# Kernel tuning notes

Hardware: AMD Instinct MI355X
Metric: run time of the kernel (lower is better)

The kernel has to match this reference:

```python
import jax, jax.numpy as jnp
import numpy as np

B, L = 4096, 200
N_USERS, N_ITEMS, N_CATS, N_DUR = 200000, 500000, 1000, 20
D = 64  # item_embed_dim == seq_embed_dim


def _lin(k, din, dout):
    kw, kb = jax.random.split(k)
    s = 1.0 / np.sqrt(din)
    return (jax.random.uniform(kw, (din, dout), minval=-s, maxval=s),
            jax.random.uniform(kb, (dout,), minval=-s, maxval=s))


def setup_inputs() -> dict:
    key = jax.random.key(0)
    ks = jax.random.split(key, 20)
    inp = {
        'user_id': jax.random.randint(ks[0], (B,), 0, N_USERS),
        'item_id': jax.random.randint(ks[1], (B,), 0, N_ITEMS),
        'item_category': jax.random.randint(ks[2], (B,), 0, N_CATS),
        'item_dur_bkt': jax.random.randint(ks[3], (B,), 0, N_DUR),
        'user_dense': jax.random.normal(ks[4], (B, 25), dtype=jnp.float32),
        'item_dense': jax.random.normal(ks[5], (B, 3), dtype=jnp.float32),
        'history_seq': jax.random.randint(ks[6], (B, L), 0, N_ITEMS + 1),
        # embedding tables (init std=0.01 as in _init_weights)
        'user_W': 0.01 * jax.random.normal(ks[7], (N_USERS, 64), dtype=jnp.float32),
        'item_W': 0.01 * jax.random.normal(ks[8], (N_ITEMS, D), dtype=jnp.float32),
        'cat_W': 0.01 * jax.random.normal(ks[9], (N_CATS, 16), dtype=jnp.float32),
        'dur_W': 0.01 * jax.random.normal(ks[10], (N_DUR, 8), dtype=jnp.float32),
        'hist_W': 0.01 * jax.random.normal(ks[11], (N_ITEMS + 1, D), dtype=jnp.float32),
    }
    # attention MLP: 4*D=256 -> 64 -> 32 -> 1
    inp['aW0'], inp['ab0'] = _lin(ks[12], 4 * D, 64)
    inp['aW1'], inp['ab1'] = _lin(ks[13], 64, 32)
    inp['aW2'], inp['ab2'] = _lin(ks[14], 32, 1)
    # final MLP: concat_dim 64+64+16+8+25+3+64 = 244 -> 256 -> 128 -> 1
    inp['mW0'], inp['mb0'] = _lin(ks[15], 244, 256)
    inp['mW1'], inp['mb1'] = _lin(ks[16], 256, 128)
    inp['mW2'], inp['mb2'] = _lin(ks[17], 128, 1)
    return inp


def reference(user_id, item_id, item_category, item_dur_bkt, user_dense, item_dense,
              history_seq, user_W, item_W, cat_W, dur_W, hist_W,
              aW0, ab0, aW1, ab1, aW2, ab2, mW0, mb0, mW1, mb1, mW2, mb2):
    u_emb = user_W[user_id]            # (B, 64)
    i_emb = item_W[item_id]            # (B, D)
    c_emb = cat_W[item_category]       # (B, 16)
    d_emb = dur_W[item_dur_bkt]        # (B, 8)
    hist = hist_W[history_seq]         # (B, L, D)

    t = i_emb[:, None, :]              # (B, 1, D); item_dim == seq_dim so no slice
    tb = jnp.broadcast_to(t, hist.shape)
    feat = jnp.concatenate([hist, tb, hist * t, hist - t], axis=-1)  # (B, L, 4D)

    h = jax.nn.relu(feat @ aW0 + ab0)
    h = jax.nn.relu(h @ aW1 + ab1)
    scores = (h @ aW2 + ab2)[..., 0]   # (B, L)

    pad_mask = history_seq == 0
    scores = jnp.where(pad_mask, jnp.float32(-1e9), scores)
    w = jax.nn.softmax(scores, axis=-1)                # (B, L)
    pooled = jnp.einsum('bl,bld->bd', w, hist)         # (B, D)

    x = jnp.concatenate([u_emb, i_emb, c_emb, d_emb, user_dense, item_dense, pooled], axis=-1)
    h = jax.nn.relu(x @ mW0 + mb0)     # dropout is identity in eval mode
    h = jax.nn.relu(h @ mW1 + mb1)
    logit = (h @ mW2 + mb2)[..., 0]
    return jax.nn.sigmoid(logit)       # (B,)
```

## Files before the change

### kernel.cpp

```cpp
#include <hip/hip_runtime.h>
#include <hip/hip_bf16.h>

#define L_SZ 200
#define RB 8
#define HS_STRIDE 72

typedef __attribute__((ext_vector_type(8))) short short8;
typedef __attribute__((ext_vector_type(4))) float floatx4;

__device__ __forceinline__ unsigned short f2bf(float f) {
    unsigned int u = __float_as_uint(f);
    unsigned int r = (u + 0x7fffu + ((u >> 16) & 1u)) >> 16;
    return (unsigned short)r;
}
__device__ __forceinline__ float bf2f(unsigned short h) {
    return __uint_as_float(((unsigned int)h) << 16);
}
__device__ __forceinline__ float wave_sum64(float v) {
    #pragma unroll
    for (int m = 1; m <= 32; m <<= 1) v += __shfl_xor(v, m, 64);
    return v;
}
__device__ __forceinline__ float wave_max64(float v) {
    #pragma unroll
    for (int m = 1; m <= 32; m <<= 1) v = fmaxf(v, __shfl_xor(v, m, 64));
    return v;
}
__device__ __forceinline__ unsigned int pk2(float a, float b) {
    return ((unsigned int)f2bf(b) << 16) | (unsigned int)f2bf(a);
}

__global__ __launch_bounds__(256, 4) void attn_kernel(
    const int* __restrict__ item_id, const int* __restrict__ hist_seq,
    const float* __restrict__ item_W, const float* __restrict__ hist_W,
    const float* __restrict__ aW0, const float* __restrict__ ab0,
    const float* __restrict__ aW1, const float* __restrict__ ab1,
    const float* __restrict__ aW2, const float* __restrict__ ab2,
    float* __restrict__ pooled_ws)
{
    __shared__ __align__(16) unsigned char smem[39136];
    unsigned short* Hs  = (unsigned short*)(smem);
    unsigned short* BB  = (unsigned short*)(smem + 28800);
    int*   seq_sh = (int*)(smem + 36992);
    float* scores = (float*)(smem + 37792);
    float* iemb   = (float*)(smem + 38592);
    float* cb     = (float*)(smem + 38848);
    float* red    = (float*)(smem + 39104);

    const int tid  = threadIdx.x;
    const int w    = tid >> 6;
    const int lane = tid & 63;
    const int b    = blockIdx.x;
    const int* hseq = hist_seq + b * L_SZ;

    if (tid < 64)   iemb[tid]   = item_W[(size_t)item_id[b] * 64 + tid];
    if (tid < L_SZ) seq_sh[tid] = hseq[tid];
    __syncthreads();

    for (int u = tid; u < L_SZ * 8; u += 256) {
        int row = u >> 3, c8 = u & 7;
        const float* src = hist_W + (size_t)seq_sh[row] * 64 + c8 * 8;
        float4 f0 = *(const float4*)src;
        float4 f1 = *(const float4*)(src + 4);
        uint4 pk;
        pk.x = pk2(f0.x, f0.y); pk.y = pk2(f0.z, f0.w);
        pk.z = pk2(f1.x, f1.y); pk.w = pk2(f1.z, f1.w);
        *(uint4*)(Hs + row * HS_STRIDE + c8 * 8) = pk;
    }
    for (int u = tid; u < 512; u += 256) {
        int j = u >> 3, k8 = u & 7;
        float v[8];
        #pragma unroll
        for (int i = 0; i < 8; ++i) {
            int k = k8 * 8 + i;
            v[i] = aW0[k * 64 + j] + aW0[(192 + k) * 64 + j]
                 + iemb[k] * aW0[(128 + k) * 64 + j];
        }
        uint4 pk;
        pk.x = pk2(v[0], v[1]); pk.y = pk2(v[2], v[3]);
        pk.z = pk2(v[4], v[5]); pk.w = pk2(v[6], v[7]);
        *(uint4*)(BB + j * 64 + (k8 ^ (j & 7)) * 8) = pk;
    }
    if (w < 2) {
        float cpart = 0.f;
        #pragma unroll 4
        for (int t = 0; t < 32; ++t) {
            int k = w * 32 + t;
            cpart = fmaf(iemb[k], aW0[(64 + k) * 64 + lane] - aW0[(192 + k) * 64 + lane], cpart);
        }
        scores[w * 64 + lane] = cpart;
    }
    const int c = lane & 15, q = lane >> 4;
    short8 bW1[2][2];
    #pragma unroll
    for (int nt = 0; nt < 2; ++nt)
        #pragma unroll
        for (int ks = 0; ks < 2; ++ks) {
            unsigned short tmp[8];
            #pragma unroll
            for (int i = 0; i < 8; ++i)
                tmp[i] = f2bf(aW1[(ks * 32 + q * 8 + i) * 32 + nt * 16 + c]);
            bW1[nt][ks] = *(short8*)tmp;
        }
    float ab1r[2], aw2r[2];
    #pragma unroll
    for (int nt = 0; nt < 2; ++nt) {
        ab1r[nt] = ab1[nt * 16 + c];
        aw2r[nt] = aW2[nt * 16 + c];
    }
    const float ab2s = ab2[0];
    __syncthreads();

    short8 bW[4][2];
    #pragma unroll
    for (int nt = 0; nt < 4; ++nt)
        #pragma unroll
        for (int ks = 0; ks < 2; ++ks)
            bW[nt][ks] = *(const short8*)(BB + (nt * 16 + c) * 64
                                             + ((4 * ks + q) ^ (c & 7)) * 8);
    if (tid < 64)
        cb[tid] = ab0[tid] + scores[tid] + scores[64 + tid];
    __syncthreads();

    float cbr[4];
    #pragma unroll
    for (int nt = 0; nt < 4; ++nt) cbr[nt] = cb[nt * 16 + c];
    unsigned short* scrw = BB + w * (16 * 64);
    const floatx4 zf = {0.f, 0.f, 0.f, 0.f};

    for (int mt = w; mt < 13; mt += 4) {
        const int rowbase = mt * 16;
        floatx4 acc0[4] = {zf, zf, zf, zf};
        #pragma unroll
        for (int ks = 0; ks < 2; ++ks) {
            short8 a = *(const short8*)(Hs + (rowbase + c) * HS_STRIDE + ks * 32 + q * 8);
            acc0[0] = __builtin_amdgcn_mfma_f32_16x16x32_bf16(a, bW[0][ks], acc0[0], 0, 0, 0);
            acc0[1] = __builtin_amdgcn_mfma_f32_16x16x32_bf16(a, bW[1][ks], acc0[1], 0, 0, 0);
            acc0[2] = __builtin_amdgcn_mfma_f32_16x16x32_bf16(a, bW[2][ks], acc0[2], 0, 0, 0);
            acc0[3] = __builtin_amdgcn_mfma_f32_16x16x32_bf16(a, bW[3][ks], acc0[3], 0, 0, 0);
        }
        #pragma unroll
        for (int nt = 0; nt < 4; ++nt)
            #pragma unroll
            for (int r = 0; r < 4; ++r) {
                float h = fmaxf(acc0[nt][r] + cbr[nt], 0.f);
                int row = q * 4 + r;
                int gp = (2 * nt + (c >> 3)) ^ (row & 7);
                scrw[row * 64 + gp * 8 + (c & 7)] = f2bf(h);
            }
        floatx4 acc1[2] = {zf, zf};
        #pragma unroll
        for (int ks = 0; ks < 2; ++ks) {
            short8 a1 = *(const short8*)(scrw + c * 64 + ((4 * ks + q) ^ (c & 7)) * 8);
            acc1[0] = __builtin_amdgcn_mfma_f32_16x16x32_bf16(a1, bW1[0][ks], acc1[0], 0, 0, 0);
            acc1[1] = __builtin_amdgcn_mfma_f32_16x16x32_bf16(a1, bW1[1][ks], acc1[1], 0, 0, 0);
        }
        float s[4];
        #pragma unroll
        for (int r = 0; r < 4; ++r)
            s[r] = fmaxf(acc1[0][r] + ab1r[0], 0.f) * aw2r[0]
                 + fmaxf(acc1[1][r] + ab1r[1], 0.f) * aw2r[1];
        #pragma unroll
        for (int m = 1; m <= 8; m <<= 1)
            #pragma unroll
            for (int r = 0; r < 4; ++r) s[r] += __shfl_xor(s[r], m, 64);
        if (c == 0) {
            #pragma unroll
            for (int r = 0; r < 4; ++r) {
                int l = rowbase + q * 4 + r;
                if (l < L_SZ)
                    scores[l] = (seq_sh[l] == 0) ? -1.0e9f : (s[r] + ab2s);
            }
        }
    }
    __syncthreads();

    float s0 = (tid < L_SZ) ? scores[tid] : -3.0e38f;
    float mx = wave_max64(s0);
    if (lane == 0) red[w] = mx;
    __syncthreads();
    mx = fmaxf(fmaxf(red[0], red[1]), fmaxf(red[2], red[3]));
    float e = (tid < L_SZ) ? __expf(s0 - mx) : 0.f;
    float sm = wave_sum64(e);
    if (lane == 0) red[4 + w] = sm;
    __syncthreads();
    const float winv = 1.f / ((red[4] + red[5]) + (red[6] + red[7]));
    if (tid < L_SZ) scores[tid] = e * winv;
    __syncthreads();

    float* pools = (float*)BB;
    {
        int g  = (w << 1) | (lane >> 5);
        int jj = lane & 31;
        int l0 = g * 26, l1 = (l0 + 26 < L_SZ) ? l0 + 26 : L_SZ;
        float p0 = 0.f, p1 = 0.f;
        for (int l = l0; l < l1; ++l) {
            float wt = scores[l];
            unsigned int pv = *(const unsigned int*)(Hs + l * HS_STRIDE + jj * 2);
            p0 = fmaf(wt, bf2f((unsigned short)(pv & 0xffffu)), p0);
            p1 = fmaf(wt, bf2f((unsigned short)(pv >> 16)), p1);
        }
        float2 pp = {p0, p1};
        *(float2*)&pools[g * 64 + jj * 2] = pp;
    }
    __syncthreads();
    if (tid < 64) {
        float sum = 0.f;
        #pragma unroll
        for (int g = 0; g < 8; ++g) sum += pools[g * 64 + tid];
        pooled_ws[(size_t)b * 64 + tid] = sum;
    }
}

__global__ __launch_bounds__(256) void mlp_kernel(
    const int* __restrict__ user_id, const int* __restrict__ item_id,
    const int* __restrict__ item_cat, const int* __restrict__ item_dur,
    const float* __restrict__ user_dense, const float* __restrict__ item_dense,
    const float* __restrict__ user_W, const float* __restrict__ item_W,
    const float* __restrict__ cat_W, const float* __restrict__ dur_W,
    const float* __restrict__ mW0, const float* __restrict__ mb0,
    const float* __restrict__ mW1, const float* __restrict__ mb1,
    const float* __restrict__ mW2, const float* __restrict__ mb2,
    const float* __restrict__ pooled_ws, float* __restrict__ out)
{
    __shared__ __align__(16) float xT[244][RB];
    __shared__ __align__(16) float h0T[256][RB];
    __shared__ __align__(16) float h1T[128][RB];
    __shared__ __align__(16) float part[128][RB];

    const int tid = threadIdx.x;
    const int b0 = blockIdx.x * RB;

    for (int idx = tid; idx < 244 * RB; idx += 256) {
        int r = idx / 244;
        int c = idx - r * 244;
        int b = b0 + r;
        float v;
        if (c < 64)       v = user_W[(size_t)user_id[b] * 64 + c];
        else if (c < 128) v = item_W[(size_t)item_id[b] * 64 + (c - 64)];
        else if (c < 144) v = cat_W[item_cat[b] * 16 + (c - 128)];
        else if (c < 152) v = dur_W[item_dur[b] * 8 + (c - 144)];
        else if (c < 177) v = user_dense[b * 25 + (c - 152)];
        else if (c < 180) v = item_dense[b * 3 + (c - 177)];
        else              v = pooled_ws[(size_t)b * 64 + (c - 180)];
        xT[c][r] = v;
    }
    __syncthreads();

    {
        float acc[RB];
        const float bias = mb0[tid];
        #pragma unroll
        for (int r = 0; r < RB; ++r) acc[r] = bias;
        #pragma unroll 4
        for (int k = 0; k < 244; ++k) {
            float wk = mW0[k * 256 + tid];
            float4 xa = *(const float4*)&xT[k][0];
            float4 xb = *(const float4*)&xT[k][4];
            acc[0] = fmaf(wk, xa.x, acc[0]);
            acc[1] = fmaf(wk, xa.y, acc[1]);
            acc[2] = fmaf(wk, xa.z, acc[2]);
            acc[3] = fmaf(wk, xa.w, acc[3]);
            acc[4] = fmaf(wk, xb.x, acc[4]);
            acc[5] = fmaf(wk, xb.y, acc[5]);
            acc[6] = fmaf(wk, xb.z, acc[6]);
            acc[7] = fmaf(wk, xb.w, acc[7]);
        }
        #pragma unroll
        for (int r = 0; r < RB; ++r) h0T[tid][r] = fmaxf(acc[r], 0.f);
    }
    __syncthreads();

    const int jj = tid & 127;
    const int half = tid >> 7;
    {
        float acc[RB];
        #pragma unroll
        for (int r = 0; r < RB; ++r) acc[r] = 0.f;
        #pragma unroll 4
        for (int t = 0; t < 128; ++t) {
            int k = half * 128 + t;
            float wk = mW1[k * 128 + jj];
            float4 ha = *(const float4*)&h0T[k][0];
            float4 hb = *(const float4*)&h0T[k][4];
            acc[0] = fmaf(wk, ha.x, acc[0]);
            acc[1] = fmaf(wk, ha.y, acc[1]);
            acc[2] = fmaf(wk, ha.z, acc[2]);
            acc[3] = fmaf(wk, ha.w, acc[3]);
            acc[4] = fmaf(wk, hb.x, acc[4]);
            acc[5] = fmaf(wk, hb.y, acc[5]);
            acc[6] = fmaf(wk, hb.z, acc[6]);
            acc[7] = fmaf(wk, hb.w, acc[7]);
        }
        if (half == 1) {
            #pragma unroll
            for (int r = 0; r < RB; ++r) part[jj][r] = acc[r];
        }
        __syncthreads();
        if (half == 0) {
            const float bias = mb1[jj];
            #pragma unroll
            for (int r = 0; r < RB; ++r)
                h1T[jj][r] = fmaxf(acc[r] + part[jj][r] + bias, 0.f);
        }
    }
    __syncthreads();

    if (tid < RB) {
        const int r = tid;
        float a0 = mb2[0], a1 = 0.f;
        #pragma unroll 8
        for (int k = 0; k < 128; k += 2) {
            a0 = fmaf(h1T[k][r],     mW2[k],     a0);
            a1 = fmaf(h1T[k + 1][r], mW2[k + 1], a1);
        }
        float a = a0 + a1;
        out[b0 + r] = 1.f / (1.f + __expf(-a));
    }
}

extern "C" void kernel_launch(void* const* d_in, const int* in_sizes, int n_in,
                              void* d_out, int out_size, void* d_ws, size_t ws_size,
                              hipStream_t stream) {
    (void)in_sizes; (void)n_in; (void)out_size; (void)ws_size;
    const int*   user_id    = (const int*)d_in[0];
    const int*   item_id    = (const int*)d_in[1];
    const int*   item_cat   = (const int*)d_in[2];
    const int*   item_dur   = (const int*)d_in[3];
    const float* user_dense = (const float*)d_in[4];
    const float* item_dense = (const float*)d_in[5];
    const int*   hist_seq   = (const int*)d_in[6];
    const float* user_W     = (const float*)d_in[7];
    const float* item_W     = (const float*)d_in[8];
    const float* cat_W      = (const float*)d_in[9];
    const float* dur_W      = (const float*)d_in[10];
    const float* hist_W     = (const float*)d_in[11];
    const float* aW0 = (const float*)d_in[12];
    const float* ab0 = (const float*)d_in[13];
    const float* aW1 = (const float*)d_in[14];
    const float* ab1 = (const float*)d_in[15];
    const float* aW2 = (const float*)d_in[16];
    const float* ab2 = (const float*)d_in[17];
    const float* mW0 = (const float*)d_in[18];
    const float* mb0 = (const float*)d_in[19];
    const float* mW1 = (const float*)d_in[20];
    const float* mb1 = (const float*)d_in[21];
    const float* mW2 = (const float*)d_in[22];
    const float* mb2 = (const float*)d_in[23];
    float* out = (float*)d_out;
    float* pooled_ws = (float*)d_ws;

    attn_kernel<<<4096, 256, 0, stream>>>(item_id, hist_seq, item_W, hist_W,
                                          aW0, ab0, aW1, ab1, aW2, ab2, pooled_ws);
    mlp_kernel<<<4096 / RB, 256, 0, stream>>>(user_id, item_id, item_cat, item_dur,
                                              user_dense, item_dense,
                                              user_W, item_W, cat_W, dur_W,
                                              mW0, mb0, mW1, mb1, mW2, mb2,
                                              pooled_ws, out);
}
```

Baseline: 433.7 us.

## Hoist per-batch attention weight prep into a prep kernel and batch gather loads

Adds a prep kernel that precomputes transposed, combined first-layer attention weights, a pre-packed bf16 MFMA fragment layout for aW1, and the per-row item bias term cb for all batch rows. The attention kernel then issues all seven hist_W gather loads up front before converting to bf16, and builds its item-dependent weight matrix from contiguous transposed tables. This removes strided aW0 reads, the per-block cb reduction and two barriers from each of 4096 blocks, and gives more memory-level parallelism in the gather. The cost is an extra kernel launch, a workspace round trip, and more registers held for the in-flight loads.

```diff
diff --git a/kernel.cpp b/kernel.cpp
--- a/kernel.cpp
+++ b/kernel.cpp
@@ -1,5 +1,4 @@
 #include <hip/hip_runtime.h>
-#include <hip/hip_bf16.h>
 
 #define L_SZ 200
 #define RB 8
@@ -30,22 +29,58 @@
     return ((unsigned int)f2bf(b) << 16) | (unsigned int)f2bf(a);
 }
 
+__global__ __launch_bounds__(256) void prep_kernel(
+    const int* __restrict__ item_id, const float* __restrict__ item_W,
+    const float* __restrict__ aW0, const float* __restrict__ ab0,
+    const float* __restrict__ aW1,
+    float* __restrict__ T1t, float* __restrict__ T2t,
+    unsigned short* __restrict__ PW1, float* __restrict__ cb_ws)
+{
+    const int tid = threadIdx.x;
+    if (blockIdx.x == 0) {
+        for (int u = tid; u < 4096; u += 256) {
+            int j = u >> 6, k = u & 63;
+            T1t[j * 64 + k] = aW0[k * 64 + j] + aW0[(192 + k) * 64 + j];
+            T2t[j * 64 + k] = aW0[(128 + k) * 64 + j];
+        }
+        for (int u = tid; u < 2048; u += 256) {
+            int i = u & 7, lane = (u >> 3) & 63, f = u >> 9;
+            int nt = f >> 1, ks = f & 1;
+            int k = ks * 32 + (lane >> 4) * 8 + i;
+            int n = nt * 16 + (lane & 15);
+            PW1[u] = f2bf(aW1[k * 32 + n]);
+        }
+    } else {
+        __shared__ float T3[64][64];
+        for (int u = tid; u < 4096; u += 256) {
+            int k = u >> 6, j = u & 63;
+            T3[k][j] = aW0[(64 + k) * 64 + j] - aW0[(192 + k) * 64 + j];
+        }
+        __syncthreads();
+        const int bl = tid >> 6, j = tid & 63;
+        const int b = (blockIdx.x - 1) * 4 + bl;
+        const float* ie = item_W + (size_t)item_id[b] * 64;
+        float acc = ab0[j];
+        #pragma unroll 8
+        for (int k = 0; k < 64; ++k) acc = fmaf(ie[k], T3[k][j], acc);
+        cb_ws[(size_t)b * 64 + j] = acc;
+    }
+}
+
 __global__ __launch_bounds__(256, 4) void attn_kernel(
     const int* __restrict__ item_id, const int* __restrict__ hist_seq,
     const float* __restrict__ item_W, const float* __restrict__ hist_W,
-    const float* __restrict__ aW0, const float* __restrict__ ab0,
-    const float* __restrict__ aW1, const float* __restrict__ ab1,
-    const float* __restrict__ aW2, const float* __restrict__ ab2,
-    float* __restrict__ pooled_ws)
+    const float* __restrict__ T1t, const float* __restrict__ T2t,
+    const unsigned short* __restrict__ PW1, const float* __restrict__ cb_ws,
+    const float* __restrict__ ab1, const float* __restrict__ aW2,
+    const float* __restrict__ ab2, float* __restrict__ pooled_ws)
 {
-    __shared__ __align__(16) unsigned char smem[39136];
+    __shared__ __align__(16) unsigned char smem[38624];
     unsigned short* Hs  = (unsigned short*)(smem);
     unsigned short* BB  = (unsigned short*)(smem + 28800);
     int*   seq_sh = (int*)(smem + 36992);
     float* scores = (float*)(smem + 37792);
-    float* iemb   = (float*)(smem + 38592);
-    float* cb     = (float*)(smem + 38848);
-    float* red    = (float*)(smem + 39104);
+    float* red    = (float*)(smem + 38592);
 
     const int tid  = threadIdx.x;
     const int w    = tid >> 6;
@@ -53,55 +88,33 @@
     const int b    = blockIdx.x;
     const int* hseq = hist_seq + b * L_SZ;
 
-    if (tid < 64)   iemb[tid]   = item_W[(size_t)item_id[b] * 64 + tid];
     if (tid < L_SZ) seq_sh[tid] = hseq[tid];
-    __syncthreads();
-
-    for (int u = tid; u < L_SZ * 8; u += 256) {
-        int row = u >> 3, c8 = u & 7;
-        const float* src = hist_W + (size_t)seq_sh[row] * 64 + c8 * 8;
-        float4 f0 = *(const float4*)src;
-        float4 f1 = *(const float4*)(src + 4);
-        uint4 pk;
-        pk.x = pk2(f0.x, f0.y); pk.y = pk2(f0.z, f0.w);
-        pk.z = pk2(f1.x, f1.y); pk.w = pk2(f1.z, f1.w);
-        *(uint4*)(Hs + row * HS_STRIDE + c8 * 8) = pk;
-    }
-    for (int u = tid; u < 512; u += 256) {
-        int j = u >> 3, k8 = u & 7;
-        float v[8];
-        #pragma unroll
-        for (int i = 0; i < 8; ++i) {
-            int k = k8 * 8 + i;
-            v[i] = aW0[k * 64 + j] + aW0[(192 + k) * 64 + j]
-                 + iemb[k] * aW0[(128 + k) * 64 + j];
-        }
-        uint4 pk;
-        pk.x = pk2(v[0], v[1]); pk.y = pk2(v[2], v[3]);
-        pk.z = pk2(v[4], v[5]); pk.w = pk2(v[6], v[7]);
-        *(uint4*)(BB + j * 64 + (k8 ^ (j & 7)) * 8) = pk;
-    }
-    if (w < 2) {
-        float cpart = 0.f;
-        #pragma unroll 4
-        for (int t = 0; t < 32; ++t) {
-            int k = w * 32 + t;
-            cpart = fmaf(iemb[k], aW0[(64 + k) * 64 + lane] - aW0[(192 + k) * 64 + lane], cpart);
-        }
-        scores[w * 64 + lane] = cpart;
-    }
+
+    const int rbase = tid >> 3, c8 = tid & 7;
+    const bool extra = tid < 64;
+    const int r6 = extra ? 192 + rbase : 0;
+    const float* sp[7];
+    #pragma unroll
+    for (int t = 0; t < 6; ++t)
+        sp[t] = hist_W + (size_t)hseq[rbase + t * 32] * 64 + c8 * 8;
+    sp[6] = hist_W + (size_t)hseq[r6] * 64 + c8 * 8;
+    float4 f0[7], f1[7];
+    #pragma unroll
+    for (int t = 0; t < 7; ++t) {
+        f0[t] = *(const float4*)sp[t];
+        f1[t] = *(const float4*)(sp[t] + 4);
+    }
+
     const int c = lane & 15, q = lane >> 4;
     short8 bW1[2][2];
     #pragma unroll
     for (int nt = 0; nt < 2; ++nt)
         #pragma unroll
-        for (int ks = 0; ks < 2; ++ks) {
-            unsigned short tmp[8];
-            #pragma unroll
-            for (int i = 0; i < 8; ++i)
-                tmp[i] = f2bf(aW1[(ks * 32 + q * 8 + i) * 32 + nt * 16 + c]);
-            bW1[nt][ks] = *(short8*)tmp;
-        }
+        for (int ks = 0; ks < 2; ++ks)
+            bW1[nt][ks] = *(const short8*)(PW1 + ((nt * 2 + ks) * 64 + lane) * 8);
+    float cbr[4];
+    #pragma unroll
+    for (int nt = 0; nt < 4; ++nt) cbr[nt] = cb_ws[(size_t)b * 64 + nt * 16 + c];
     float ab1r[2], aw2r[2];
     #pragma unroll
     for (int nt = 0; nt < 2; ++nt) {
@@ -109,6 +122,44 @@
         aw2r[nt] = aW2[nt * 16 + c];
     }
     const float ab2s = ab2[0];
+
+    #pragma unroll
+    for (int t = 0; t < 6; ++t) {
+        uint4 pk;
+        pk.x = pk2(f0[t].x, f0[t].y); pk.y = pk2(f0[t].z, f0[t].w);
+        pk.z = pk2(f1[t].x, f1[t].y); pk.w = pk2(f1[t].z, f1[t].w);
+        *(uint4*)(Hs + (rbase + t * 32) * HS_STRIDE + c8 * 8) = pk;
+    }
+    if (extra) {
+        uint4 pk;
+        pk.x = pk2(f0[6].x, f0[6].y); pk.y = pk2(f0[6].z, f0[6].w);
+        pk.z = pk2(f1[6].x, f1[6].y); pk.w = pk2(f1[6].z, f1[6].w);
+        *(uint4*)(Hs + r6 * HS_STRIDE + c8 * 8) = pk;
+    }
+
+    {
+        const float* irow = item_W + (size_t)item_id[b] * 64;
+        const int j0 = tid >> 3;
+        float4 em0 = *(const float4*)(irow + c8 * 8);
+        float4 em1 = *(const float4*)(irow + c8 * 8 + 4);
+        #pragma unroll
+        for (int t = 0; t < 2; ++t) {
+            int j = j0 + t * 32;
+            const float* p1 = T1t + j * 64 + c8 * 8;
+            const float* p2 = T2t + j * 64 + c8 * 8;
+            float4 a0 = *(const float4*)p1, a1 = *(const float4*)(p1 + 4);
+            float4 b0 = *(const float4*)p2, b1 = *(const float4*)(p2 + 4);
+            float v[8];
+            v[0] = a0.x + em0.x * b0.x; v[1] = a0.y + em0.y * b0.y;
+            v[2] = a0.z + em0.z * b0.z; v[3] = a0.w + em0.w * b0.w;
+            v[4] = a1.x + em1.x * b1.x; v[5] = a1.y + em1.y * b1.y;
+            v[6] = a1.z + em1.z * b1.z; v[7] = a1.w + em1.w * b1.w;
+            uint4 pk;
+            pk.x = pk2(v[0], v[1]); pk.y = pk2(v[2], v[3]);
+            pk.z = pk2(v[4], v[5]); pk.w = pk2(v[6], v[7]);
+            *(uint4*)(BB + j * 64 + (c8 ^ (j & 7)) * 8) = pk;
+        }
+    }
     __syncthreads();
 
     short8 bW[4][2];
@@ -118,13 +169,8 @@
         for (int ks = 0; ks < 2; ++ks)
             bW[nt][ks] = *(const short8*)(BB + (nt * 16 + c) * 64
                                              + ((4 * ks + q) ^ (c & 7)) * 8);
-    if (tid < 64)
-        cb[tid] = ab0[tid] + scores[tid] + scores[64 + tid];
-    __syncthreads();
-
-    float cbr[4];
-    #pragma unroll
-    for (int nt = 0; nt < 4; ++nt) cbr[nt] = cb[nt * 16 + c];
+    __syncthreads();
+
     unsigned short* scrw = BB + w * (16 * 64);
     const floatx4 zf = {0.f, 0.f, 0.f, 0.f};
 
@@ -348,10 +394,19 @@
     const float* mW2 = (const float*)d_in[22];
     const float* mb2 = (const float*)d_in[23];
     float* out = (float*)d_out;
-    float* pooled_ws = (float*)d_ws;
-
+
+    char* ws = (char*)d_ws;
+    float* pooled_ws = (float*)ws;
+    float* cb_ws     = (float*)(ws + (1u << 20));
+    float* T1t       = (float*)(ws + (2u << 20));
+    float* T2t       = (float*)(ws + (2u << 20) + 16384);
+    unsigned short* PW1 = (unsigned short*)(ws + (2u << 20) + 32768);
+
+    prep_kernel<<<1025, 256, 0, stream>>>(item_id, item_W, aW0, ab0, aW1,
+                                          T1t, T2t, PW1, cb_ws);
     attn_kernel<<<4096, 256, 0, stream>>>(item_id, hist_seq, item_W, hist_W,
-                                          aW0, ab0, aW1, ab1, aW2, ab2, pooled_ws);
+                                          T1t, T2t, PW1, cb_ws,
+                                          ab1, aW2, ab2, pooled_ws);
     mlp_kernel<<<4096 / RB, 256, 0, stream>>>(user_id, item_id, item_cat, item_dur,
                                               user_dense, item_dense,
                                               user_W, item_W, cat_W, dur_W,
```

Result: faster. 389.8 us (-10.1%).
